# Optimization experiments

Hardware: AMD Instinct MI355X
Metric: run time of the kernel (lower is better)

The kernel has to match this reference:

```python
import jax, jax.numpy as jnp
import numpy as np

B, D_IN, H, V_TOT, T = 131072, 128, 256, 6, 6  # total_vocab = vocab_size+1 = 6


def setup_inputs() -> dict:
    key = jax.random.key(0)
    ks = jax.random.split(key, 16)
    s = 0.02
    return {
        "x": jax.random.normal(ks[0], (B, D_IN), jnp.float32),
        "W_enc": jax.random.normal(ks[1], (D_IN, H), jnp.float32) * s,
        "b_enc": jnp.zeros((H,), jnp.float32),
        "W_embed": jax.random.normal(ks[2], (V_TOT, H), jnp.float32) * s,
        "b_embed": jnp.zeros((H,), jnp.float32),
        "W_z": jax.random.normal(ks[3], (2 * H, H), jnp.float32) * s,
        "b_z": jnp.zeros((H,), jnp.float32),
        "W_r": jax.random.normal(ks[4], (2 * H, H), jnp.float32) * s,
        "b_r": jnp.zeros((H,), jnp.float32),
        "W_h": jax.random.normal(ks[5], (2 * H, H), jnp.float32) * s,
        "b_h": jnp.zeros((H,), jnp.float32),
        "W_out": jax.random.normal(ks[6], (H, V_TOT), jnp.float32) * s,
        "b_out": jnp.zeros((V_TOT,), jnp.float32),
        "start_embed": jax.random.normal(ks[7], (H,), jnp.float32) * 0.01,
    }


def reference(x, W_enc, b_enc, W_embed, b_embed, W_z, b_z, W_r, b_r, W_h, b_h,
              W_out, b_out, start_embed):
    h0 = x @ W_enc + b_enc                      # encoder: (B, H)
    bsz = h0.shape[0]
    keys = jax.random.split(jax.random.key(42), T)

    def gru(xin, h):
        c = jnp.concatenate([xin, h], axis=-1)
        z = jax.nn.sigmoid(c @ W_z + b_z)
        r = jax.nn.sigmoid(c @ W_r + b_r)
        cr = jnp.concatenate([xin, r * h], axis=-1)
        h_t = jnp.tanh(cr @ W_h + b_h)
        return (1 - z) * h + z * h_t

    def step(carry, key_t):
        h, prev_embed, total_lp, stopped, lengths = carry
        h = gru(prev_embed, h)
        logits = h @ W_out + b_out              # (B, V_TOT)
        token = jax.random.categorical(key_t, logits)  # training=True sampling
        logp = jax.nn.log_softmax(logits)
        active = (~stopped).astype(logits.dtype)
        lp = jnp.take_along_axis(logp, token[:, None], axis=1)[:, 0] * active
        total_lp = total_lp + lp
        onehot = jax.nn.one_hot(token, V_TOT, dtype=logits.dtype) * active[:, None]
        is_stop = token == (V_TOT - 1)
        lengths = lengths + ((~stopped) & (~is_stop)).astype(jnp.int32)
        stopped = stopped | is_stop
        prev_embed = jax.lax.stop_gradient(onehot) @ W_embed + b_embed
        return (h, prev_embed, total_lp, stopped, lengths), onehot

    init = (h0,
            jnp.broadcast_to(start_embed, (bsz, H)),
            jnp.zeros((bsz,), h0.dtype),
            jnp.zeros((bsz,), bool),
            jnp.zeros((bsz,), jnp.int32))
    (h, _, total_log_prob, _, lengths), onehots = jax.lax.scan(step, init, keys)
    # onehots: (T, B, V_TOT) -> message (B, T*V_TOT)
    message = jnp.transpose(onehots, (1, 0, 2)).reshape(bsz, T * V_TOT)
    return message, total_log_prob, lengths
```

## Files before the change

### kernel.cpp

```cpp
#include <hip/hip_runtime.h>
#include <stdint.h>

#define NB   131072
#define DIN  128
#define HD   256
#define VT   6
#define TS   6
#define BM   32
#define NTH  512
#define MT   2

typedef __attribute__((ext_vector_type(8))) short bfrag;
typedef __attribute__((ext_vector_type(4))) short bh4;
typedef __attribute__((ext_vector_type(4))) float f32x4;

struct Keys { uint32_t a[6]; uint32_t b[6]; };

#define HPS(p, kc, nt, lp, j) ((((p) * 8 + (kc)) * 1040) + (nt) * 512 + (lp) * 8 + (j))

__host__ __device__ inline void tf2x32(uint32_t k0, uint32_t k1,
                                       uint32_t c0, uint32_t c1,
                                       uint32_t& o0, uint32_t& o1) {
  uint32_t ks2 = k0 ^ k1 ^ 0x1BD11BDAu;
  uint32_t x0 = c0 + k0, x1 = c1 + k1;
#define TFR(d) { x0 += x1; x1 = (x1 << (d)) | (x1 >> (32 - (d))); x1 ^= x0; }
  TFR(13) TFR(15) TFR(26) TFR(6)
  x0 += k1;  x1 += ks2 + 1u;
  TFR(17) TFR(29) TFR(16) TFR(24)
  x0 += ks2; x1 += k0 + 2u;
  TFR(13) TFR(15) TFR(26) TFR(6)
  x0 += k0;  x1 += k1 + 3u;
  TFR(17) TFR(29) TFR(16) TFR(24)
  x0 += k1;  x1 += ks2 + 4u;
  TFR(13) TFR(15) TFR(26) TFR(6)
  x0 += ks2; x1 += k0 + 5u;
#undef TFR
  o0 = x0; o1 = x1;
}

__device__ __forceinline__ unsigned short f2bf(float x) {
  uint32_t b = __float_as_uint(x);
  uint32_t r = b + 0x7FFFu + ((b >> 16) & 1u);
  return (unsigned short)(r >> 16);
}
__device__ __forceinline__ float bf2f(unsigned short u) {
  return __uint_as_float(((uint32_t)u) << 16);
}
__device__ __forceinline__ float sigf(float v) { return 1.0f / (1.0f + expf(-v)); }

#define MFMA16(a, b, c) __builtin_amdgcn_mfma_f32_16x16x32_bf16((a), (b), (c), 0, 0, 0)

__device__ __forceinline__ f32x4 prod6(const bfrag A[3], bfrag B0, bfrag B1, bfrag B2,
                                       f32x4 c) {
  c = MFMA16(A[0], B0, c);
  c = MFMA16(A[0], B1, c);
  c = MFMA16(A[1], B0, c);
  c = MFMA16(A[1], B1, c);
  c = MFMA16(A[0], B2, c);
  c = MFMA16(A[2], B0, c);
  return c;
}

__global__ void pre_kernel(const float* __restrict__ W_enc,
                           const float* __restrict__ W_embed,
                           const float* __restrict__ b_embed,
                           const float* __restrict__ start_embed,
                           const float* __restrict__ W_z, const float* __restrict__ b_z,
                           const float* __restrict__ W_r, const float* __restrict__ b_r,
                           const float* __restrict__ W_h, const float* __restrict__ b_h,
                           const float* __restrict__ W_out,
                           float* __restrict__ pre,
                           unsigned short* __restrict__ encf,
                           unsigned short* __restrict__ zf,
                           unsigned short* __restrict__ rf,
                           unsigned short* __restrict__ hf,
                           unsigned short* __restrict__ woutf) {
  const int bid = blockIdx.x;
  if (bid < 24) {
    __shared__ float xin[HD];
    const int c = bid & 7, g = bid >> 3, j = threadIdx.x;
    float v;
    if (c < 6)       v = W_embed[c * HD + j] + b_embed[j];
    else if (c == 6) v = b_embed[j];
    else             v = start_embed[j];
    xin[j] = v;
    __syncthreads();
    const float* Wg = (g == 0) ? W_z : (g == 1) ? W_r : W_h;
    const float* bg = (g == 0) ? b_z : (g == 1) ? b_r : b_h;
    float acc = bg[j];
    for (int k = 0; k < HD; ++k) acc += xin[k] * Wg[k * HD + j];
    pre[(g * 8 + c) * HD + j] = acc;
    return;
  }
  if (bid >= 136) {
    int id2 = (bid - 136) * 256 + threadIdx.x;
    int kc = id2 >> 6, lane = id2 & 63;
    int m = lane & 15, k0 = kc * 32 + ((lane >> 4) & 3) * 8;
    __align__(16) unsigned short P[3][8];
#pragma unroll
    for (int j = 0; j < 8; ++j) {
      float w = (m < VT) ? W_out[(size_t)(k0 + j) * VT + m] : 0.f;
      unsigned short h1 = f2bf(w);  float r1 = w - bf2f(h1);
      unsigned short h2 = f2bf(r1); float r2 = r1 - bf2f(h2);
      P[0][j] = h1; P[1][j] = h2; P[2][j] = f2bf(r2);
    }
    for (int p = 0; p < 3; ++p) {
      unsigned short* d = woutf + ((size_t)(p * 8 + kc) * 512) + (size_t)lane * 8;
      *(uint4*)d = *(const uint4*)P[p];
    }
    return;
  }
  int id = (bid - 24) * 256 + threadIdx.x;
  const float* src; unsigned short* dst; int kc, mt, lane, KC, krow0;
  if (id < 4096) {
    lane = id & 63; mt = (id >> 6) & 15; kc = id >> 10;
    src = W_enc; dst = encf; KC = 4; krow0 = 0;
  } else {
    int rem = id - 4096; int g = rem >> 13; int rr = rem & 8191;
    lane = rr & 63; mt = (rr >> 6) & 15; kc = rr >> 10;
    src = (g == 0) ? W_z : (g == 1) ? W_r : W_h;
    dst = (g == 0) ? zf  : (g == 1) ? rf  : hf;
    KC = 8; krow0 = 256;
  }
  const int m  = mt * 16 + (lane & 15);
  const int k0 = kc * 32 + ((lane >> 4) & 3) * 8;
  __align__(16) unsigned short P[3][8];
#pragma unroll
  for (int j = 0; j < 8; ++j) {
    float w = src[(size_t)(krow0 + k0 + j) * HD + m];
    unsigned short h1 = f2bf(w);  float r1 = w - bf2f(h1);
    unsigned short h2 = f2bf(r1); float r2 = r1 - bf2f(h2);
    P[0][j] = h1; P[1][j] = h2; P[2][j] = f2bf(r2);
  }
  for (int p = 0; p < 3; ++p) {
    unsigned short* d = dst + ((size_t)(p * KC + kc) * 16 + mt) * 512 + (size_t)lane * 8;
    *(uint4*)d = *(const uint4*)P[p];
  }
}

template<int KC, int NG>
__device__ __forceinline__ void gemm_pass(const unsigned short* __restrict__ f0,
                                          const unsigned short* __restrict__ f1,
                                          const unsigned short* hp_s,
                                          int wave, int lane,
                                          f32x4 acc0[MT][2], f32x4 acc1[MT][2]) {
#pragma unroll 1
  for (int kc = 0; kc < KC; ++kc) {
    bfrag B[3][2];
#pragma unroll
    for (int p = 0; p < 3; ++p)
#pragma unroll
      for (int nt = 0; nt < 2; ++nt)
        B[p][nt] = *(const bfrag*)&hp_s[HPS(p, kc, nt, lane, 0)];
#pragma unroll
    for (int mtl = 0; mtl < MT; ++mtl) {
      const int fo = (kc * 16 + wave * MT + mtl) * 512 + lane * 8;
      bfrag A0[3], A1[3];
#pragma unroll
      for (int p = 0; p < 3; ++p) A0[p] = *(const bfrag*)(f0 + fo + p * (KC * 8192));
      if (NG == 2) {
#pragma unroll
        for (int p = 0; p < 3; ++p) A1[p] = *(const bfrag*)(f1 + fo + p * (KC * 8192));
      }
#pragma unroll
      for (int nt = 0; nt < 2; ++nt) {
        acc0[mtl][nt] = prod6(A0, B[0][nt], B[1][nt], B[2][nt], acc0[mtl][nt]);
        if (NG == 2)
          acc1[mtl][nt] = prod6(A1, B[0][nt], B[1][nt], B[2][nt], acc1[mtl][nt]);
      }
    }
  }
}

__device__ __forceinline__ void gen_gumbel(float* __restrict__ gmb, int s, int b0,
                                           int tile, int lane,
                                           uint32_t ka, uint32_t kb) {
  uint32_t basej = (uint32_t)(b0 + tile * 16) * 6u;
#pragma unroll
  for (int rep = 0; rep < 2; ++rep) {
    int d = rep * 64 + lane;
    if (d < 96) {
      uint32_t o0, o1;
      tf2x32(ka, kb, 0u, basej + (uint32_t)d, o0, o1);
      uint32_t bits = o0 ^ o1;
      float f = __uint_as_float((bits >> 9) | 0x3f800000u) - 1.0f;
      float u = (f > 0.f) ? f : 1.175494350822288e-38f;
      float lg1 = (float)log((double)u);
      float lg2 = (float)log((double)(-lg1));
      gmb[((s & 1) * 32 + tile * 16 + d / 6) * 6 + (d % 6)] = -lg2;
    }
  }
}

__launch_bounds__(NTH, 4)
__global__ void main_kernel(const float* __restrict__ x,
                            const float* __restrict__ b_enc,
                            const float* __restrict__ b_out,
                            const float* __restrict__ pre,
                            const unsigned short* __restrict__ encf,
                            const unsigned short* __restrict__ zf,
                            const unsigned short* __restrict__ rf,
                            const unsigned short* __restrict__ hf,
                            const unsigned short* __restrict__ woutf,
                            float* __restrict__ out, Keys keys) {
  __shared__ __align__(16) unsigned short hp_s[3 * 8 * 1040];
  __shared__ float gmb_s[2 * 32 * 6];
  __shared__ float boutL[16];
  __shared__ unsigned state[BM];
  __shared__ float tlp[BM];

  const int tid = threadIdx.x;
  const int wave = tid >> 6, lane = tid & 63;
  const int ln = lane & 15, qk = lane >> 4;
  const int b0 = blockIdx.x * BM;

  if (tid < 16) boutL[tid] = (tid < VT) ? b_out[tid] : 0.f;
  if (tid < BM) { state[tid] = 7u; tlp[tid] = 0.f; }

  for (int i = tid; i < BM * DIN; i += NTH) {
    int row = i >> 7, k = i & 127;
    float v = x[(size_t)(b0 + row) * DIN + k];
    unsigned short h1 = f2bf(v);  float r1 = v - bf2f(h1);
    unsigned short h2 = f2bf(r1); float r2 = r1 - bf2f(h2);
    int kc = k >> 5, nt = row >> 4, lp = (row & 15) + 16 * ((k >> 3) & 3), j = k & 7;
    hp_s[HPS(0, kc, nt, lp, j)] = h1;
    hp_s[HPS(1, kc, nt, lp, j)] = h2;
    hp_s[HPS(2, kc, nt, lp, j)] = f2bf(r2);
  }
  if (wave == 2 || wave == 3)
    gen_gumbel(gmb_s, 0, b0, wave - 2, lane, keys.a[0], keys.b[0]);
  __syncthreads();

  f32x4 acc0[MT][2], acc1[MT][2], z_s[MT][2], hold[MT][2];

#pragma unroll
  for (int mtl = 0; mtl < MT; ++mtl) {
    int mb = (wave * MT + mtl) * 16 + qk * 4;
    f32x4 be = *(const f32x4*)&b_enc[mb];
#pragma unroll
    for (int nt = 0; nt < 2; ++nt) acc0[mtl][nt] = be;
  }
  gemm_pass<4, 1>(encf, nullptr, hp_s, wave, lane, acc0, acc1);
  __syncthreads();
#pragma unroll
  for (int mtl = 0; mtl < MT; ++mtl) {
    int mb = (wave * MT + mtl) * 16 + qk * 4;
    int kc = mb >> 5, hi2 = (mb >> 3) & 3, j0 = mb & 7, lp = ln + 16 * hi2;
#pragma unroll
    for (int nt = 0; nt < 2; ++nt) {
      f32x4 o = acc0[mtl][nt];
      hold[mtl][nt] = o;
      bh4 P0, P1, P2;
#pragma unroll
      for (int j = 0; j < 4; ++j) {
        float v = o[j];
        unsigned short h1 = f2bf(v);  float r1 = v - bf2f(h1);
        unsigned short h2 = f2bf(r1); float r2 = r1 - bf2f(h2);
        P0[j] = (short)h1; P1[j] = (short)h2; P2[j] = (short)f2bf(r2);
      }
      *(bh4*)&hp_s[HPS(0, kc, nt, lp, j0)] = P0;
      *(bh4*)&hp_s[HPS(1, kc, nt, lp, j0)] = P1;
      *(bh4*)&hp_s[HPS(2, kc, nt, lp, j0)] = P2;
    }
  }
  __syncthreads();

#pragma unroll 1
  for (int t = 0; t < TS; ++t) {
#pragma unroll
    for (int mtl = 0; mtl < MT; ++mtl) {
      int mb = (wave * MT + mtl) * 16 + qk * 4;
#pragma unroll
      for (int nt = 0; nt < 2; ++nt) {
        int code = (int)(state[nt * 16 + ln] & 7u);
        acc0[mtl][nt] = *(const f32x4*)&pre[(0 * 8 + code) * 256 + mb];
        acc1[mtl][nt] = *(const f32x4*)&pre[(1 * 8 + code) * 256 + mb];
      }
    }
    gemm_pass<8, 2>(zf, rf, hp_s, wave, lane, acc0, acc1);
    __syncthreads();
#pragma unroll
    for (int mtl = 0; mtl < MT; ++mtl) {
      int mb = (wave * MT + mtl) * 16 + qk * 4;
      int kc = mb >> 5, hi2 = (mb >> 3) & 3, j0 = mb & 7, lp = ln + 16 * hi2;
#pragma unroll
      for (int nt = 0; nt < 2; ++nt) {
        f32x4 ho = hold[mtl][nt];
        f32x4 zv;
        bh4 P0, P1, P2;
#pragma unroll
        for (int j = 0; j < 4; ++j) {
          zv[j] = sigf(acc0[mtl][nt][j]);
          float rhv = sigf(acc1[mtl][nt][j]) * ho[j];
          unsigned short h1 = f2bf(rhv); float r1 = rhv - bf2f(h1);
          unsigned short h2 = f2bf(r1);  float r2 = r1 - bf2f(h2);
          P0[j] = (short)h1; P1[j] = (short)h2; P2[j] = (short)f2bf(r2);
        }
        z_s[mtl][nt] = zv;
        *(bh4*)&hp_s[HPS(0, kc, nt, lp, j0)] = P0;
        *(bh4*)&hp_s[HPS(1, kc, nt, lp, j0)] = P1;
        *(bh4*)&hp_s[HPS(2, kc, nt, lp, j0)] = P2;
      }
    }
    __syncthreads();

#pragma unroll
    for (int mtl = 0; mtl < MT; ++mtl) {
      int mb = (wave * MT + mtl) * 16 + qk * 4;
#pragma unroll
      for (int nt = 0; nt < 2; ++nt) {
        int code = (int)(state[nt * 16 + ln] & 7u);
        acc0[mtl][nt] = *(const f32x4*)&pre[(2 * 8 + code) * 256 + mb];
      }
    }
    gemm_pass<8, 1>(hf, nullptr, hp_s, wave, lane, acc0, acc1);
    __syncthreads();
#pragma unroll
    for (int mtl = 0; mtl < MT; ++mtl) {
      int mb = (wave * MT + mtl) * 16 + qk * 4;
      int kc = mb >> 5, hi2 = (mb >> 3) & 3, j0 = mb & 7, lp = ln + 16 * hi2;
#pragma unroll
      for (int nt = 0; nt < 2; ++nt) {
        f32x4 z = z_s[mtl][nt], ho = hold[mtl][nt], hn;
        bh4 P0, P1, P2;
#pragma unroll
        for (int j = 0; j < 4; ++j) {
          float ht = tanhf(acc0[mtl][nt][j]);
          hn[j] = (1.0f - z[j]) * ho[j] + z[j] * ht;
          unsigned short h1 = f2bf(hn[j]); float r1 = hn[j] - bf2f(h1);
          unsigned short h2 = f2bf(r1);    float r2 = r1 - bf2f(h2);
          P0[j] = (short)h1; P1[j] = (short)h2; P2[j] = (short)f2bf(r2);
        }
        hold[mtl][nt] = hn;
        *(bh4*)&hp_s[HPS(0, kc, nt, lp, j0)] = P0;
        *(bh4*)&hp_s[HPS(1, kc, nt, lp, j0)] = P1;
        *(bh4*)&hp_s[HPS(2, kc, nt, lp, j0)] = P2;
      }
    }
    __syncthreads();

    if (wave < 2) {
      f32x4 lacc;
#pragma unroll
      for (int j = 0; j < 4; ++j) lacc[j] = boutL[qk * 4 + j];
#pragma unroll 1
      for (int kc = 0; kc < 8; ++kc) {
        bfrag B0 = *(const bfrag*)&hp_s[HPS(0, kc, wave, lane, 0)];
        bfrag B1 = *(const bfrag*)&hp_s[HPS(1, kc, wave, lane, 0)];
        bfrag B2 = *(const bfrag*)&hp_s[HPS(2, kc, wave, lane, 0)];
        bfrag A[3];
#pragma unroll
        for (int p = 0; p < 3; ++p)
          A[p] = *(const bfrag*)(woutf + (p * 8 + kc) * 512 + lane * 8);
        lacc = prod6(A, B0, B1, B2, lacc);
      }
      float l4 = __shfl(lacc[0], ln + 16, 64);
      float l5 = __shfl(lacc[1], ln + 16, 64);
      if (qk == 0) {
        const int m = wave * 16 + ln;
        const int row = b0 + m;
        unsigned st = state[m];
        if (!(st & 8u)) {
          float l[VT] = {lacc[0], lacc[1], lacc[2], lacc[3], l4, l5};
          float best = 0.f; int tok = 0;
#pragma unroll
          for (int v = 0; v < VT; ++v) {
            float val = l[v] + gmb_s[((t & 1) * 32 + m) * 6 + v];
            if (v == 0 || val > best) { best = val; tok = v; }
          }
          float lmax = l[0];
#pragma unroll
          for (int v = 1; v < VT; ++v) lmax = fmaxf(lmax, l[v]);
          float s = 0.f;
#pragma unroll
          for (int v = 0; v < VT; ++v) s += expf(l[v] - lmax);
          float lp = (l[tok] - lmax) - logf(s);
          tlp[m] += lp;
          const bool is_stop = (tok == VT - 1);
          unsigned len = ((st >> 4) & 7u) + (is_stop ? 0u : 1u);
#pragma unroll
          for (int v = 0; v < VT; ++v)
            out[(size_t)row * (TS * VT) + t * VT + v] = (v == tok) ? 1.0f : 0.0f;
          state[m] = (unsigned)tok | (is_stop ? 8u : 0u) | (len << 4);
        } else {
#pragma unroll
          for (int v = 0; v < VT; ++v)
            out[(size_t)row * (TS * VT) + t * VT + v] = 0.0f;
          state[m] = 6u | 8u | (st & 0x70u);
        }
      }
    } else if ((wave == 2 || wave == 3) && t + 1 < TS) {
      gen_gumbel(gmb_s, t + 1, b0, wave - 2, lane, keys.a[t + 1], keys.b[t + 1]);
    }
    __syncthreads();
  }

  if (tid < BM) {
    const int row = b0 + tid;
    out[(size_t)NB * (TS * VT) + row]      = tlp[tid];
    out[(size_t)NB * (TS * VT) + NB + row] = (float)((state[tid] >> 4) & 7u);
  }
}

extern "C" void kernel_launch(void* const* d_in, const int* in_sizes, int n_in,
                              void* d_out, int out_size, void* d_ws, size_t ws_size,
                              hipStream_t stream) {
  (void)in_sizes; (void)n_in; (void)out_size; (void)ws_size;
  const float* x          = (const float*)d_in[0];
  const float* W_enc      = (const float*)d_in[1];
  const float* b_enc      = (const float*)d_in[2];
  const float* W_embed    = (const float*)d_in[3];
  const float* b_embed    = (const float*)d_in[4];
  const float* W_z        = (const float*)d_in[5];
  const float* b_z        = (const float*)d_in[6];
  const float* W_r        = (const float*)d_in[7];
  const float* b_r        = (const float*)d_in[8];
  const float* W_h        = (const float*)d_in[9];
  const float* b_h        = (const float*)d_in[10];
  const float* W_out      = (const float*)d_in[11];
  const float* b_out      = (const float*)d_in[12];
  const float* start_embed= (const float*)d_in[13];
  float* out = (float*)d_out;

  float* pre = (float*)d_ws;
  unsigned short* encf = (unsigned short*)((char*)d_ws + 24576);
  unsigned short* zfb  = (unsigned short*)((char*)d_ws + 221184);
  unsigned short* rfb  = (unsigned short*)((char*)d_ws + 614400);
  unsigned short* hfb  = (unsigned short*)((char*)d_ws + 1007616);
  unsigned short* wof  = (unsigned short*)((char*)d_ws + 1400832);

  pre_kernel<<<138, 256, 0, stream>>>(W_enc, W_embed, b_embed, start_embed,
                                      W_z, b_z, W_r, b_r, W_h, b_h, W_out,
                                      pre, encf, zfb, rfb, hfb, wof);

  Keys K;
  for (int t = 0; t < 6; ++t) {
    uint32_t o0, o1;
    tf2x32(0u, 42u, 0u, (uint32_t)t, o0, o1);
    K.a[t] = o0; K.b[t] = o1;
  }

  main_kernel<<<NB / BM, NTH, 0, stream>>>(x, b_enc, b_out,
                                           pre, encf, zfb, rfb, hfb, wof, out, K);
}
```

Measured before the change: 1.968 ms.

## Double-buffer hidden-state LDS tiles to drop per-phase barriers

Splits the shared-memory hidden-state fragment buffer into two ping-pong buffers, so each GEMM pass reads one buffer while the epilogue writes the other. This removes the __syncthreads after the encoder, z/r and h GEMMs. The candidate-gate bias preload is hoisted next to the z/r preload into a separate accumulator. The cost is double the LDS footprint (about 100KB), and launch bounds drop to 2 blocks per SM, which lowers occupancy and adds register pressure from the extra accumulator.

```diff
diff --git a/kernel.cpp b/kernel.cpp
--- a/kernel.cpp
+++ b/kernel.cpp
@@ -17,6 +17,7 @@
 struct Keys { uint32_t a[6]; uint32_t b[6]; };
 
 #define HPS(p, kc, nt, lp, j) ((((p) * 8 + (kc)) * 1040) + (nt) * 512 + (lp) * 8 + (j))
+#define HPSZ (3 * 8 * 1040)
 
 __host__ __device__ inline void tf2x32(uint32_t k0, uint32_t k1,
                                        uint32_t c0, uint32_t c1,
@@ -141,7 +142,7 @@
 template<int KC, int NG>
 __device__ __forceinline__ void gemm_pass(const unsigned short* __restrict__ f0,
                                           const unsigned short* __restrict__ f1,
-                                          const unsigned short* hp_s,
+                                          const unsigned short* hp,
                                           int wave, int lane,
                                           f32x4 acc0[MT][2], f32x4 acc1[MT][2]) {
 #pragma unroll 1
@@ -151,7 +152,7 @@
     for (int p = 0; p < 3; ++p)
 #pragma unroll
       for (int nt = 0; nt < 2; ++nt)
-        B[p][nt] = *(const bfrag*)&hp_s[HPS(p, kc, nt, lane, 0)];
+        B[p][nt] = *(const bfrag*)&hp[HPS(p, kc, nt, lane, 0)];
 #pragma unroll
     for (int mtl = 0; mtl < MT; ++mtl) {
       const int fo = (kc * 16 + wave * MT + mtl) * 512 + lane * 8;
@@ -192,7 +193,7 @@
   }
 }
 
-__launch_bounds__(NTH, 4)
+__launch_bounds__(NTH, 2)
 __global__ void main_kernel(const float* __restrict__ x,
                             const float* __restrict__ b_enc,
                             const float* __restrict__ b_out,
@@ -203,7 +204,7 @@
                             const unsigned short* __restrict__ hf,
                             const unsigned short* __restrict__ woutf,
                             float* __restrict__ out, Keys keys) {
-  __shared__ __align__(16) unsigned short hp_s[3 * 8 * 1040];
+  __shared__ __align__(16) unsigned short hp2[2][HPSZ];
   __shared__ float gmb_s[2 * 32 * 6];
   __shared__ float boutL[16];
   __shared__ unsigned state[BM];
@@ -223,15 +224,15 @@
     unsigned short h1 = f2bf(v);  float r1 = v - bf2f(h1);
     unsigned short h2 = f2bf(r1); float r2 = r1 - bf2f(h2);
     int kc = k >> 5, nt = row >> 4, lp = (row & 15) + 16 * ((k >> 3) & 3), j = k & 7;
-    hp_s[HPS(0, kc, nt, lp, j)] = h1;
-    hp_s[HPS(1, kc, nt, lp, j)] = h2;
-    hp_s[HPS(2, kc, nt, lp, j)] = f2bf(r2);
+    hp2[0][HPS(0, kc, nt, lp, j)] = h1;
+    hp2[0][HPS(1, kc, nt, lp, j)] = h2;
+    hp2[0][HPS(2, kc, nt, lp, j)] = f2bf(r2);
   }
   if (wave == 2 || wave == 3)
     gen_gumbel(gmb_s, 0, b0, wave - 2, lane, keys.a[0], keys.b[0]);
   __syncthreads();
 
-  f32x4 acc0[MT][2], acc1[MT][2], z_s[MT][2], hold[MT][2];
+  f32x4 acc0[MT][2], acc1[MT][2], accH[MT][2], z_s[MT][2], hold[MT][2];
 
 #pragma unroll
   for (int mtl = 0; mtl < MT; ++mtl) {
@@ -240,8 +241,7 @@
 #pragma unroll
     for (int nt = 0; nt < 2; ++nt) acc0[mtl][nt] = be;
   }
-  gemm_pass<4, 1>(encf, nullptr, hp_s, wave, lane, acc0, acc1);
-  __syncthreads();
+  gemm_pass<4, 1>(encf, nullptr, hp2[0], wave, lane, acc0, acc1);
 #pragma unroll
   for (int mtl = 0; mtl < MT; ++mtl) {
     int mb = (wave * MT + mtl) * 16 + qk * 4;
@@ -258,9 +258,9 @@
         unsigned short h2 = f2bf(r1); float r2 = r1 - bf2f(h2);
         P0[j] = (short)h1; P1[j] = (short)h2; P2[j] = (short)f2bf(r2);
       }
-      *(bh4*)&hp_s[HPS(0, kc, nt, lp, j0)] = P0;
-      *(bh4*)&hp_s[HPS(1, kc, nt, lp, j0)] = P1;
-      *(bh4*)&hp_s[HPS(2, kc, nt, lp, j0)] = P2;
+      *(bh4*)&hp2[1][HPS(0, kc, nt, lp, j0)] = P0;
+      *(bh4*)&hp2[1][HPS(1, kc, nt, lp, j0)] = P1;
+      *(bh4*)&hp2[1][HPS(2, kc, nt, lp, j0)] = P2;
     }
   }
   __syncthreads();
@@ -275,10 +275,10 @@
         int code = (int)(state[nt * 16 + ln] & 7u);
         acc0[mtl][nt] = *(const f32x4*)&pre[(0 * 8 + code) * 256 + mb];
         acc1[mtl][nt] = *(const f32x4*)&pre[(1 * 8 + code) * 256 + mb];
-      }
-    }
-    gemm_pass<8, 2>(zf, rf, hp_s, wave, lane, acc0, acc1);
-    __syncthreads();
+        accH[mtl][nt] = *(const f32x4*)&pre[(2 * 8 + code) * 256 + mb];
+      }
+    }
+    gemm_pass<8, 2>(zf, rf, hp2[1], wave, lane, acc0, acc1);
 #pragma unroll
     for (int mtl = 0; mtl < MT; ++mtl) {
       int mb = (wave * MT + mtl) * 16 + qk * 4;
@@ -297,24 +297,14 @@
           P0[j] = (short)h1; P1[j] = (short)h2; P2[j] = (short)f2bf(r2);
         }
         z_s[mtl][nt] = zv;
-        *(bh4*)&hp_s[HPS(0, kc, nt, lp, j0)] = P0;
-        *(bh4*)&hp_s[HPS(1, kc, nt, lp, j0)] = P1;
-        *(bh4*)&hp_s[HPS(2, kc, nt, lp, j0)] = P2;
+        *(bh4*)&hp2[0][HPS(0, kc, nt, lp, j0)] = P0;
+        *(bh4*)&hp2[0][HPS(1, kc, nt, lp, j0)] = P1;
+        *(bh4*)&hp2[0][HPS(2, kc, nt, lp, j0)] = P2;
       }
     }
     __syncthreads();
 
-#pragma unroll
-    for (int mtl = 0; mtl < MT; ++mtl) {
-      int mb = (wave * MT + mtl) * 16 + qk * 4;
-#pragma unroll
-      for (int nt = 0; nt < 2; ++nt) {
-        int code = (int)(state[nt * 16 + ln] & 7u);
-        acc0[mtl][nt] = *(const f32x4*)&pre[(2 * 8 + code) * 256 + mb];
-      }
-    }
-    gemm_pass<8, 1>(hf, nullptr, hp_s, wave, lane, acc0, acc1);
-    __syncthreads();
+    gemm_pass<8, 1>(hf, nullptr, hp2[0], wave, lane, accH, acc1);
 #pragma unroll
     for (int mtl = 0; mtl < MT; ++mtl) {
       int mb = (wave * MT + mtl) * 16 + qk * 4;
@@ -325,16 +315,16 @@
         bh4 P0, P1, P2;
 #pragma unroll
         for (int j = 0; j < 4; ++j) {
-          float ht = tanhf(acc0[mtl][nt][j]);
+          float ht = tanhf(accH[mtl][nt][j]);
           hn[j] = (1.0f - z[j]) * ho[j] + z[j] * ht;
           unsigned short h1 = f2bf(hn[j]); float r1 = hn[j] - bf2f(h1);
           unsigned short h2 = f2bf(r1);    float r2 = r1 - bf2f(h2);
           P0[j] = (short)h1; P1[j] = (short)h2; P2[j] = (short)f2bf(r2);
         }
         hold[mtl][nt] = hn;
-        *(bh4*)&hp_s[HPS(0, kc, nt, lp, j0)] = P0;
-        *(bh4*)&hp_s[HPS(1, kc, nt, lp, j0)] = P1;
-        *(bh4*)&hp_s[HPS(2, kc, nt, lp, j0)] = P2;
+        *(bh4*)&hp2[1][HPS(0, kc, nt, lp, j0)] = P0;
+        *(bh4*)&hp2[1][HPS(1, kc, nt, lp, j0)] = P1;
+        *(bh4*)&hp2[1][HPS(2, kc, nt, lp, j0)] = P2;
       }
     }
     __syncthreads();
@@ -345,9 +335,9 @@
       for (int j = 0; j < 4; ++j) lacc[j] = boutL[qk * 4 + j];
 #pragma unroll 1
       for (int kc = 0; kc < 8; ++kc) {
-        bfrag B0 = *(const bfrag*)&hp_s[HPS(0, kc, wave, lane, 0)];
-        bfrag B1 = *(const bfrag*)&hp_s[HPS(1, kc, wave, lane, 0)];
-        bfrag B2 = *(const bfrag*)&hp_s[HPS(2, kc, wave, lane, 0)];
+        bfrag B0 = *(const bfrag*)&hp2[1][HPS(0, kc, wave, lane, 0)];
+        bfrag B1 = *(const bfrag*)&hp2[1][HPS(1, kc, wave, lane, 0)];
+        bfrag B2 = *(const bfrag*)&hp2[1][HPS(2, kc, wave, lane, 0)];
         bfrag A[3];
 #pragma unroll
         for (int p = 0; p < 3; ++p)
```

Measured after the change: 2.139 ms. 1.09x slower.
